# Kernel tuning notes

Measured on AMD Instinct MI355X. Metric: run time of the kernel, lower is better.

## Reference

```python
import jax, jax.numpy as jnp
import numpy as np

B, L, C = 4, 4096, 2048
NH, K = 32, 16
F = C // NH  # head_dim = 64
LR = 1.0     # config.inner_net_lr
EPS = 1e-6


def setup_inputs() -> dict:
    key = jax.random.key(0)
    ks = jax.random.split(key, 8)
    s = 0.02
    return {
        "hidden_states": jax.random.normal(ks[0], (B, L, C), jnp.float32),
        "q_w": jax.random.normal(ks[1], (C, C), jnp.float32) * s,
        "k_w": jax.random.normal(ks[2], (C, C), jnp.float32) * s,
        "v_w": jax.random.normal(ks[3], (C, C), jnp.float32) * s,
        "o_w": jax.random.normal(ks[4], (C, C), jnp.float32) * s,
        "lin_w": jax.random.normal(ks[5], (NH, 1, C), jnp.float32) * s,
        "lin_b": jnp.zeros((NH, 1), jnp.float32),
        "ln_w": jnp.ones((NH, F), jnp.float32),
        "ln_b": jnp.zeros((NH, F), jnp.float32),
        "W1": jax.random.normal(ks[6], (NH, F, F), jnp.float32) * s,
        "b1": jnp.zeros((NH, 1, F), jnp.float32),
    }


def _ln(z, g, b):
    # LayerNormFunction.forward over last dim (head_dim)
    mu = z.mean(-1, keepdims=True)
    var = jnp.mean((z - mu) ** 2, axis=-1, keepdims=True)
    x_hat = (z - mu) * jax.lax.rsqrt(var + EPS)
    return g * x_hat + b


def _ln_l2_bwd(z, target, g, b):
    # decoder_ln_bwd: grad of 0.5*||LN(z) - target||^2 w.r.t. z, fused LN fwd+bwd
    mu = z.mean(-1, keepdims=True)
    var = jnp.mean((z - mu) ** 2, axis=-1, keepdims=True)
    std = jnp.sqrt(var + EPS)
    x_hat = (z - mu) / std
    gy = (g * x_hat + b - target) * g  # grad_x_hat
    return (F * gy - gy.sum(-1, keepdims=True)
            - x_hat * (gy * x_hat).sum(-1, keepdims=True)) / (F * std)


def reference(hidden_states, q_w, k_w, v_w, o_w, lin_w, lin_b, ln_w, ln_b, W1, b1):
    nc = L // K  # number of inner chunks

    def proj(w):
        x = hidden_states @ w.T                      # [B,L,C]
        x = x.reshape(B, nc, K, NH, F)
        return jnp.moveaxis(x, 3, 1)                 # [B,NH,nc,K,F]

    XC, XB, XA = proj(q_w), proj(k_w), proj(v_w)

    # per-head ilr gate: vmap(F.linear) over heads, softplus activation
    Xr = hidden_states.reshape(B, nc, K, C)
    ilr = jax.nn.softplus(jnp.einsum('bnkc,hoc->bhnko', Xr, lin_w)
                          + lin_b[None, :, None, None, :])   # [B,NH,nc,K,1]
    token_idx = 1.0 / jnp.arange(1, K + 1, dtype=jnp.float32)
    coeff = (LR * token_idx)[None, None, None, :, None] * ilr / F  # [B,NH,nc,K,1]

    gamma = ln_w[None, :, None, :]  # [1,NH,1,F]
    beta = ln_b[None, :, None, :]
    mask = jnp.tril(jnp.ones((K, K), jnp.float32))

    W1_0 = jnp.broadcast_to(W1[None], (B, NH, F, F))
    b1_0 = jnp.broadcast_to(b1[None], (B, NH, 1, F))

    def step(carry, xs):
        W1s, b1s = carry
        xa, xb, xc, co = xs                 # [B,NH,K,F], co: [B,NH,K,1]
        Z1 = xb @ W1s + b1s                 # inner-net forward
        gZ = _ln_l2_bwd(Z1, xa - xb, gamma, beta)  # grad_l_wrt_Z1
        Attn1 = (xc @ jnp.swapaxes(xb, -1, -2)) * mask      # tril(XC XB^T) [B,NH,K,K]
        b1_bar = b1s - (co * mask) @ gZ                      # [B,NH,K,F]
        Z1_bar = xc @ W1s - (co * Attn1) @ gZ + b1_bar       # dual-form output
        co_last = co[:, :, -1:, :]                           # [B,NH,1,1]
        W1_new = W1s - jnp.swapaxes(co_last * xb, -1, -2) @ gZ
        b1_new = b1_bar[:, :, -1:, :]
        xcw = xc + _ln(Z1_bar, gamma, beta)
        return (W1_new, b1_new), xcw

    xs = tuple(jnp.moveaxis(t, 2, 0) for t in (XA, XB, XC, coeff))
    _, out = jax.lax.scan(step, (W1_0, b1_0), xs)   # out: [nc,B,NH,K,F]
    out = jnp.moveaxis(out, 0, 1)                    # [B,nc,NH,K,F]
    out = jnp.swapaxes(out, 2, 3).reshape(B, L, C)   # [B,L,C]
    return out @ o_w.T
```

## Files before the change

### kernel.cpp

```cpp
#include <hip/hip_runtime.h>
#include <hip/hip_bf16.h>

#define B_ 4
#define L_ 4096
#define C_ 2048
#define NH_ 32
#define K_ 16
#define F_ 64
#define NC_ 256
#define EPS_ 1e-6f

typedef _Float16 half8 __attribute__((ext_vector_type(8)));
typedef _Float16 half4 __attribute__((ext_vector_type(4)));
typedef float f32x4 __attribute__((ext_vector_type(4)));

__device__ __forceinline__ float red16(float v) {
  int x;
  x = __builtin_amdgcn_update_dpp(0, __builtin_bit_cast(int, v), 0xB1, 0xF, 0xF, true);
  v += __builtin_bit_cast(float, x);
  x = __builtin_amdgcn_update_dpp(0, __builtin_bit_cast(int, v), 0x4E, 0xF, 0xF, true);
  v += __builtin_bit_cast(float, x);
  x = __builtin_amdgcn_update_dpp(0, __builtin_bit_cast(int, v), 0x124, 0xF, 0xF, true);
  v += __builtin_bit_cast(float, x);
  x = __builtin_amdgcn_update_dpp(0, __builtin_bit_cast(int, v), 0x128, 0xF, 0xF, true);
  v += __builtin_bit_cast(float, x);
  return v;
}

__device__ __forceinline__ void gl_lds16(const _Float16* g, _Float16* l) {
  __builtin_amdgcn_global_load_lds(
      (const __attribute__((address_space(1))) void*)g,
      (__attribute__((address_space(3))) void*)l, 16, 0, 0);
}

__global__ __launch_bounds__(256) void cast_f16(const float* __restrict__ in,
                                                _Float16* __restrict__ out, int n8) {
  int i = blockIdx.x * 256 + threadIdx.x;
  if (i >= n8) return;
  const float4* ip = (const float4*)in;
  float4 a = ip[2*i], b = ip[2*i+1];
  half8 o;
  o[0]=(_Float16)a.x; o[1]=(_Float16)a.y; o[2]=(_Float16)a.z; o[3]=(_Float16)a.w;
  o[4]=(_Float16)b.x; o[5]=(_Float16)b.y; o[6]=(_Float16)b.z; o[7]=(_Float16)b.w;
  ((half8*)out)[i] = o;
}

#define GBM2 256
#define GBN2 256
#define GBK2 32

template<typename OT>
__global__ __launch_bounds__(512) void gemm_f16_v2(
    const _Float16* __restrict__ A, const _Float16* __restrict__ Bm,
    OT* __restrict__ C, int M, int N, int Kd)
{
  __shared__ __align__(16) _Float16 As[3][GBM2*GBK2];
  __shared__ __align__(16) _Float16 Bs[3][GBM2*GBK2];
  const int t = threadIdx.x;
  const int lane = t & 63;
  const int w = t >> 6;
  const int bn = blockIdx.x, bm = blockIdx.y;
  const int wm = (w >> 2) * 128;
  const int wn = (w & 3) * 64;
  const int ln = lane & 15, q = lane >> 4;

  const _Float16* gA0 = A  + ((long)(bm*GBM2 +        (t>>2)))*Kd + (t&3)*8;
  const _Float16* gA1 = A  + ((long)(bm*GBM2 + 128 +  (t>>2)))*Kd + (t&3)*8;
  const _Float16* gB0 = Bm + ((long)(bn*GBN2 +        (t>>2)))*Kd + (t&3)*8;
  const _Float16* gB1 = Bm + ((long)(bn*GBN2 + 128 +  (t>>2)))*Kd + (t&3)*8;

  auto stage = [&](int tile, int bi) {
    const long off = (long)tile * GBK2;
    gl_lds16(gA0 + off, &As[bi][(size_t)t*8]);
    gl_lds16(gA1 + off, &As[bi][(size_t)(t+512)*8]);
    gl_lds16(gB0 + off, &Bs[bi][(size_t)t*8]);
    gl_lds16(gB1 + off, &Bs[bi][(size_t)(t+512)*8]);
  };

  f32x4 acc[8][4];
#pragma unroll
  for (int i = 0; i < 8; ++i)
#pragma unroll
    for (int j = 0; j < 4; ++j) acc[i][j] = (f32x4){0.f,0.f,0.f,0.f};

  auto compute = [&](int kt) {
    const _Float16* as = As[kt % 3];
    const _Float16* bs = Bs[kt % 3];
    half8 bf[4];
#pragma unroll
    for (int ni = 0; ni < 4; ++ni)
      bf[ni] = *(const half8*)(bs + (size_t)(wn + ni*16 + ln)*GBK2 + q*8);
    __builtin_amdgcn_s_setprio(1);
#pragma unroll
    for (int mi = 0; mi < 8; ++mi) {
      half8 af = *(const half8*)(as + (size_t)(wm + mi*16 + ln)*GBK2 + q*8);
#pragma unroll
      for (int ni = 0; ni < 4; ++ni)
        acc[mi][ni] = __builtin_amdgcn_mfma_f32_16x16x32_f16(af, bf[ni], acc[mi][ni], 0, 0, 0);
    }
    __builtin_amdgcn_s_setprio(0);
  };

  const int NT = Kd / GBK2;
  stage(0, 0);
  stage(1, 1);

  for (int kt = 0; kt < NT - 2; ++kt) {
    __builtin_amdgcn_sched_barrier(0);
    __builtin_amdgcn_s_barrier();
    __builtin_amdgcn_sched_barrier(0);
    stage(kt + 2, (kt + 2) % 3);
    __builtin_amdgcn_sched_barrier(0);
    asm volatile("s_waitcnt vmcnt(8)" ::: "memory");
    __builtin_amdgcn_sched_barrier(0);
    compute(kt);
  }
  __builtin_amdgcn_sched_barrier(0);
  __builtin_amdgcn_s_barrier();
  __builtin_amdgcn_sched_barrier(0);
  asm volatile("s_waitcnt vmcnt(4)" ::: "memory");
  __builtin_amdgcn_sched_barrier(0);
  compute(NT - 2);
  __builtin_amdgcn_sched_barrier(0);
  __builtin_amdgcn_s_barrier();
  __builtin_amdgcn_sched_barrier(0);
  asm volatile("s_waitcnt vmcnt(0)" ::: "memory");
  __builtin_amdgcn_sched_barrier(0);
  compute(NT - 1);

  const int cr = q * 4, cc = ln;
#pragma unroll
  for (int mi = 0; mi < 8; ++mi)
#pragma unroll
    for (int ni = 0; ni < 4; ++ni)
#pragma unroll
      for (int r = 0; r < 4; ++r) {
        long row = (long)bm*GBM2 + wm + mi*16 + cr + r;
        long col = (long)bn*GBN2 + wn + ni*16 + cc;
        C[row*(long)N + col] = (OT)acc[mi][ni][r];
      }
}

__global__ __launch_bounds__(256) void ilr_kernel(
    const float* __restrict__ hid, const float* __restrict__ lin_w,
    const float* __restrict__ lin_b, float* __restrict__ coeff)
{
  const int t = threadIdx.x;
  const int lane = t & 63;
  const int w = t >> 6;
  const int row0 = blockIdx.x * 16 + w * 4;

  float4 hv[4][8];
#pragma unroll
  for (int r = 0; r < 4; ++r) {
    const float* hp = hid + (size_t)(row0 + r) * C_;
#pragma unroll
    for (int i = 0; i < 8; ++i) hv[r][i] = *(const float4*)(hp + i*256 + lane*4);
  }
  float res[4] = {0.f,0.f,0.f,0.f};
  for (int h = 0; h < NH_; ++h) {
    const float* wp = lin_w + (size_t)h * C_;
    float s[4] = {0.f,0.f,0.f,0.f};
#pragma unroll
    for (int i = 0; i < 8; ++i) {
      float4 wv = *(const float4*)(wp + i*256 + lane*4);
#pragma unroll
      for (int r = 0; r < 4; ++r)
        s[r] += hv[r][i].x*wv.x + hv[r][i].y*wv.y + hv[r][i].z*wv.z + hv[r][i].w*wv.w;
    }
#pragma unroll
    for (int o = 32; o > 0; o >>= 1)
#pragma unroll
      for (int r = 0; r < 4; ++r) s[r] += __shfl_xor(s[r], o, 64);
    if (lane == h) { res[0]=s[0]; res[1]=s[1]; res[2]=s[2]; res[3]=s[3]; }
  }
  if (lane < NH_) {
    float lb = lin_b[lane];
#pragma unroll
    for (int r = 0; r < 4; ++r) {
      int row = row0 + r;
      int b = row >> 12;
      int li = row & (L_ - 1);
      int k = li & (K_ - 1);
      float x = res[r] + lb;
      float sp = (x > 20.f) ? x : log1pf(expf(x));
      float v = (1.0f / (float)(k + 1)) * sp * (1.0f / (float)F_);
      coeff[((size_t)(b * NH_ + lane)) * L_ + li] = v;
    }
  }
}

struct Ck2 {
  half4 xbA[4], xsA[4];
  float co4[4], co15;
};

__device__ __forceinline__ void load_ck2(
    Ck2& c, const _Float16* Kp, const _Float16* S, const float* co,
    size_t rowbase, int hoff, size_t cobase, int n, int q, int ln)
{
#pragma unroll
  for (int kt = 0; kt < 4; ++kt) {
    size_t idx = (rowbase + ln) * C_ + hoff + 16*kt + 4*q;
    c.xbA[kt] = *(const half4*)(Kp + idx);
    c.xsA[kt] = *(const half4*)(S  + idx);
  }
#pragma unroll
  for (int r = 0; r < 4; ++r) c.co4[r] = co[cobase + (size_t)n*K_ + 4*q + r];
  c.co15 = co[cobase + (size_t)n*K_ + 15];
}

__global__ __launch_bounds__(128, 1) void scan_kernel(
    const _Float16* __restrict__ Q, const _Float16* __restrict__ Kp,
    const _Float16* __restrict__ V,
    const float* __restrict__ coeff, const float* __restrict__ W1g, const float* __restrict__ b1g,
    const float* __restrict__ ln_w, const float* __restrict__ ln_b,
    _Float16* __restrict__ OF)
{
  const int bh = blockIdx.x;
  const int b = bh >> 5, h = bh & 31;
  const int tid = threadIdx.x;
  const int lane = tid & 63;
  const bool isP = tid < 64;
  const int q = lane >> 4, ln = lane & 15;
  const int hoff = h * F_;
  const size_t cobase = (size_t)bh * L_;
  const size_t brow = (size_t)b * L_;

  __shared__ half4 gzs[4][4][64];

  half4 W1f[4][4];
#pragma unroll
  for (int kt = 0; kt < 4; ++kt)
#pragma unroll
    for (int t = 0; t < 4; ++t) {
      half4 hv;
#pragma unroll
      for (int j = 0; j < 4; ++j)
        hv[j] = (_Float16)W1g[(size_t)h*F_*F_ + (size_t)(16*kt + 4*q + j)*F_ + 16*t + ln];
      W1f[kt][t] = hv;
    }
  float b1r[4], gamt[4], bett[4];
#pragma unroll
  for (int t = 0; t < 4; ++t) {
    b1r[t]  = b1g[hoff + 16*t + ln];
    gamt[t] = ln_w[hoff + 16*t + ln];
    bett[t] = ln_b[hoff + 16*t + ln];
  }
  half4 maskA, maskI;
#pragma unroll
  for (int j = 0; j < 4; ++j) {
    maskA[j] = (_Float16)((4*q + j <= ln) ? 1.f : 0.f);
    maskI[j] = (_Float16)((4*q + j == ln) ? 1.f : 0.f);
  }
  const f32x4 zf4 = (f32x4){0.f, 0.f, 0.f, 0.f};

  const _Float16* S = isP ? V : Q;

  auto iter = [&](int i, Ck2& cur, Ck2& nxt) {
    half4 gzf[4];
    half4 xbTp[4];
    float co15p = 0.f;

    if (isP) {
      if (i < NC_) {
        co15p = cur.co15;
        if (i + 1 < NC_)
          load_ck2(nxt, Kp, S, coeff, brow + (size_t)(i+1)*K_, hoff, cobase, i+1, q, ln);
        f32x4 tgD[4];
#pragma unroll
        for (int t = 0; t < 4; ++t) {
          half4 dd = cur.xsA[t] - cur.xbA[t];
          tgD[t] = __builtin_amdgcn_mfma_f32_16x16x16f16(dd, maskI, zf4, 0, 0, 0);
          f32x4 x = __builtin_amdgcn_mfma_f32_16x16x16f16(cur.xbA[t], maskI, zf4, 0, 0, 0);
          half4 v;
#pragma unroll
          for (int r = 0; r < 4; ++r) v[r] = (_Float16)x[r];
          xbTp[t] = v;
        }
        f32x4 za[4];
#pragma unroll
        for (int t = 0; t < 4; ++t) {
          f32x4 zh = (f32x4){b1r[t], b1r[t], b1r[t], b1r[t]};
#pragma unroll
          for (int kt = 0; kt < 4; ++kt)
            zh = __builtin_amdgcn_mfma_f32_16x16x16f16(cur.xbA[kt], W1f[kt][t], zh, 0, 0, 0);
          za[t] = zh;
        }
#pragma unroll
        for (int r = 0; r < 4; ++r) {
          float zr[4], s1 = 0.f, s2 = 0.f;
#pragma unroll
          for (int t = 0; t < 4; ++t) { zr[t] = za[t][r]; s1 += zr[t]; s2 += zr[t]*zr[t]; }
          s1 = red16(s1); s2 = red16(s2);
          float mu = s1 * (1.f/F_);
          float istd = rsqrtf(s2 * (1.f/F_) - mu*mu + EPS_);
          float xh[4], gy[4], sg = 0.f, sx = 0.f;
#pragma unroll
          for (int t = 0; t < 4; ++t) {
            xh[t] = (zr[t] - mu) * istd;
            gy[t] = (gamt[t]*xh[t] + bett[t] - tgD[t][r]) * gamt[t];
            sg += gy[t]; sx += gy[t]*xh[t];
          }
          sg = red16(sg); sx = red16(sx);
          const float sc = istd * (1.f/F_);
#pragma unroll
          for (int t = 0; t < 4; ++t)
            gzf[t][r] = (_Float16)((F_*gy[t] - sg - xh[t]*sx) * sc);
        }
#pragma unroll
        for (int t = 0; t < 4; ++t) gzs[i & 3][t][lane] = gzf[t];
      }
    } else {
      if (i < NC_)
        load_ck2(nxt, Kp, S, coeff, brow + (size_t)i*K_, hoff, cobase, i, q, ln);
    }

    __syncthreads();

    if (isP) {
      if (i < NC_) {
        f32x4 cum3[4];
#pragma unroll
        for (int t = 0; t < 4; ++t)
          cum3[t] = __builtin_amdgcn_mfma_f32_16x16x16f16(maskA, gzf[t], zf4, 0, 0, 0);
#pragma unroll
        for (int t = 0; t < 4; ++t) {
          float tmp = b1r[t] - co15p * cum3[t][3];
          b1r[t] = __shfl(tmp, 48 + ln, 64);
        }
#pragma unroll
        for (int mt = 0; mt < 4; ++mt)
#pragma unroll
          for (int t = 0; t < 4; ++t) {
            f32x4 d = __builtin_amdgcn_mfma_f32_16x16x16f16(xbTp[mt], gzf[t], zf4, 0, 0, 0);
            half4 dt;
#pragma unroll
            for (int r = 0; r < 4; ++r) dt[r] = (_Float16)(co15p * d[r]);
            W1f[mt][t] = W1f[mt][t] - dt;
          }
      }
    } else {
      if (i > 0) {
        const int jc = i - 1;
        const size_t rowbase = brow + (size_t)jc * K_;
        half4 gz[4];
#pragma unroll
        for (int t = 0; t < 4; ++t) gz[t] = gzs[jc & 3][t][lane];
        f32x4 xcsD[4]; half4 xbT[4];
#pragma unroll
        for (int t = 0; t < 4; ++t) {
          xcsD[t] = __builtin_amdgcn_mfma_f32_16x16x16f16(cur.xsA[t], maskI, zf4, 0, 0, 0);
          f32x4 x = __builtin_amdgcn_mfma_f32_16x16x16f16(cur.xbA[t], maskI, zf4, 0, 0, 0);
          half4 v;
#pragma unroll
          for (int r = 0; r < 4; ++r) v[r] = (_Float16)x[r];
          xbT[t] = v;
        }
        f32x4 at0 = zf4, at1 = zf4;
        at0 = __builtin_amdgcn_mfma_f32_16x16x16f16(cur.xbA[0], cur.xsA[0], at0, 0, 0, 0);
        at0 = __builtin_amdgcn_mfma_f32_16x16x16f16(cur.xbA[1], cur.xsA[1], at0, 0, 0, 0);
        at1 = __builtin_amdgcn_mfma_f32_16x16x16f16(cur.xbA[2], cur.xsA[2], at1, 0, 0, 0);
        at1 = __builtin_amdgcn_mfma_f32_16x16x16f16(cur.xbA[3], cur.xsA[3], at1, 0, 0, 0);
        f32x4 at = at0 + at1;
        half4 atf;
#pragma unroll
        for (int r = 0; r < 4; ++r) atf[r] = (_Float16)((4*q + r <= ln) ? at[r] : 0.f);
        f32x4 cum[4], ag[4];
#pragma unroll
        for (int t = 0; t < 4; ++t) {
          cum[t] = __builtin_amdgcn_mfma_f32_16x16x16f16(maskA, gz[t], zf4, 0, 0, 0);
          ag[t]  = __builtin_amdgcn_mfma_f32_16x16x16f16(atf,   gz[t], zf4, 0, 0, 0);
        }
        float zbf[4][4];
#pragma unroll
        for (int t = 0; t < 4; ++t) {
          f32x4 zh = zf4;
#pragma unroll
          for (int kt = 0; kt < 4; ++kt)
            zh = __builtin_amdgcn_mfma_f32_16x16x16f16(cur.xsA[kt], W1f[kt][t], zh, 0, 0, 0);
#pragma unroll
          for (int r = 0; r < 4; ++r)
            zbf[t][r] = zh[r] + b1r[t] - cur.co4[r]*(ag[t][r] + cum[t][r]);
        }
#pragma unroll
        for (int r = 0; r < 4; ++r) {
          float zr[4], s1 = 0.f, s2 = 0.f;
#pragma unroll
          for (int t = 0; t < 4; ++t) { zr[t] = zbf[t][r]; s1 += zr[t]; s2 += zr[t]*zr[t]; }
          s1 = red16(s1); s2 = red16(s2);
          float mu = s1 * (1.f/F_);
          float istd = rsqrtf(s2 * (1.f/F_) - mu*mu + EPS_);
#pragma unroll
          for (int t = 0; t < 4; ++t) {
            float ov = xcsD[t][r] + gamt[t]*((zr[t] - mu)*istd) + bett[t];
            OF[(rowbase + 4*q + r) * C_ + hoff + 16*t + ln] = (_Float16)ov;
          }
        }
#pragma unroll
        for (int t = 0; t < 4; ++t) {
          float tmp = b1r[t] - cur.co15 * cum[t][3];
          b1r[t] = __shfl(tmp, 48 + ln, 64);
        }
#pragma unroll
        for (int mt = 0; mt < 4; ++mt)
#pragma unroll
          for (int t = 0; t < 4; ++t) {
            f32x4 d = __builtin_amdgcn_mfma_f32_16x16x16f16(xbT[mt], gz[t], zf4, 0, 0, 0);
            half4 dt;
#pragma unroll
            for (int r = 0; r < 4; ++r) dt[r] = (_Float16)(cur.co15 * d[r]);
            W1f[mt][t] = W1f[mt][t] - dt;
          }
      }
    }
  };

  Ck2 cka, ckb;
  if (isP) load_ck2(cka, Kp, S, coeff, brow, hoff, cobase, 0, q, ln);

  for (int i = 0; i < NC_; i += 2) {
    iter(i,     cka, ckb);
    iter(i + 1, ckb, cka);
  }
  iter(NC_, cka, ckb);
}

extern "C" void kernel_launch(void* const* d_in, const int* in_sizes, int n_in,
                              void* d_out, int out_size, void* d_ws, size_t ws_size,
                              hipStream_t stream)
{
  const float* hid   = (const float*)d_in[0];
  const float* q_w   = (const float*)d_in[1];
  const float* k_w   = (const float*)d_in[2];
  const float* v_w   = (const float*)d_in[3];
  const float* o_w   = (const float*)d_in[4];
  const float* lin_w = (const float*)d_in[5];
  const float* lin_b = (const float*)d_in[6];
  const float* ln_w  = (const float*)d_in[7];
  const float* ln_b  = (const float*)d_in[8];
  const float* W1    = (const float*)d_in[9];
  const float* b1    = (const float*)d_in[10];
  float* out = (float*)d_out;

  const size_t BLC = (size_t)B_ * L_ * C_;
  const size_t CC  = (size_t)C_ * C_;
  _Float16* HF = (_Float16*)d_ws;
  _Float16* WF = HF + BLC;
  _Float16* KF = WF + CC;
  _Float16* VF = KF + BLC;
  float*    CO = (float*)(VF + BLC);
  _Float16* QF = (_Float16*)d_out;

  const int M = B_ * L_, N = C_, Kd = C_;
  dim3 gg2(N / GBN2, M / GBM2);
  const int n8h = (int)(BLC / 8);
  const int n8w = (int)(CC / 8);

  cast_f16<<<(n8h+255)/256, 256, 0, stream>>>(hid, HF, n8h);
  cast_f16<<<(n8w+255)/256, 256, 0, stream>>>(q_w, WF, n8w);
  gemm_f16_v2<_Float16><<<gg2, 512, 0, stream>>>(HF, WF, QF, M, N, Kd);
  cast_f16<<<(n8w+255)/256, 256, 0, stream>>>(k_w, WF, n8w);
  gemm_f16_v2<_Float16><<<gg2, 512, 0, stream>>>(HF, WF, KF, M, N, Kd);
  cast_f16<<<(n8w+255)/256, 256, 0, stream>>>(v_w, WF, n8w);
  gemm_f16_v2<_Float16><<<gg2, 512, 0, stream>>>(HF, WF, VF, M, N, Kd);
  ilr_kernel<<<M / 16, 256, 0, stream>>>(hid, lin_w, lin_b, CO);
  scan_kernel<<<B_ * NH_, 128, 0, stream>>>(QF, KF, VF, CO, W1, b1, ln_w, ln_b, HF);
  cast_f16<<<(n8w+255)/256, 256, 0, stream>>>(o_w, WF, n8w);
  gemm_f16_v2<float><<<gg2, 512, 0, stream>>>(HF, WF, out, M, N, Kd);
}
```

Baseline: 1.379 ms.

## Fuse QKV projections into one GEMM with BK=64 swizzled double-buffered pipeline

Concatenates the three fp16-cast projection weights and runs a single GEMM over a 3x-wide N grid, routing each column block to the Q, K or V output. The GEMM kernel moves from a triple-buffered BK=32 loop to a double-buffered BK=64 loop with XOR-swizzled LDS layout, split staging interleaved between MFMA phases, and a launch bound requesting two blocks per CU. The aim is fewer launches, a larger grid for better CU fill, fewer LDS bank conflicts and better overlap of loads with compute. In exchange it costs more workspace for the concatenated weights, and the higher occupancy target may cause register pressure.

```diff
diff --git a/kernel.cpp b/kernel.cpp
--- a/kernel.cpp
+++ b/kernel.cpp
@@ -45,37 +45,37 @@
   ((half8*)out)[i] = o;
 }
 
-#define GBM2 256
-#define GBN2 256
-#define GBK2 32
+#define BM3 256
+#define BN3 256
+#define BK3 64
 
 template<typename OT>
-__global__ __launch_bounds__(512) void gemm_f16_v2(
+__global__ __launch_bounds__(512, 2) void gemm_f16_v3(
     const _Float16* __restrict__ A, const _Float16* __restrict__ Bm,
-    OT* __restrict__ C, int M, int N, int Kd)
+    OT* __restrict__ C0, OT* __restrict__ C1, OT* __restrict__ C2, int Kd)
 {
-  __shared__ __align__(16) _Float16 As[3][GBM2*GBK2];
-  __shared__ __align__(16) _Float16 Bs[3][GBM2*GBK2];
+  __shared__ __align__(16) _Float16 As[2][2][128*64];
+  __shared__ __align__(16) _Float16 Bs[2][2][128*64];
   const int t = threadIdx.x;
   const int lane = t & 63;
   const int w = t >> 6;
+  const int wr = w >> 2, wc = w & 3;
   const int bn = blockIdx.x, bm = blockIdx.y;
-  const int wm = (w >> 2) * 128;
-  const int wn = (w & 3) * 64;
   const int ln = lane & 15, q = lane >> 4;
 
-  const _Float16* gA0 = A  + ((long)(bm*GBM2 +        (t>>2)))*Kd + (t&3)*8;
-  const _Float16* gA1 = A  + ((long)(bm*GBM2 + 128 +  (t>>2)))*Kd + (t&3)*8;
-  const _Float16* gB0 = Bm + ((long)(bn*GBN2 +        (t>>2)))*Kd + (t&3)*8;
-  const _Float16* gB1 = Bm + ((long)(bn*GBN2 + 128 +  (t>>2)))*Kd + (t&3)*8;
-
-  auto stage = [&](int tile, int bi) {
-    const long off = (long)tile * GBK2;
-    gl_lds16(gA0 + off, &As[bi][(size_t)t*8]);
-    gl_lds16(gA1 + off, &As[bi][(size_t)(t+512)*8]);
-    gl_lds16(gB0 + off, &Bs[bi][(size_t)t*8]);
-    gl_lds16(gB1 + off, &Bs[bi][(size_t)(t+512)*8]);
+  const int srow = t >> 3, sc = t & 7;
+  const int clg = sc ^ (2 * ((srow >> 2) & 1));
+
+  auto stageA = [&](int kt, int h, int db) {
+    const _Float16* g = A + ((long)(bm*BM3 + h*128 + srow))*Kd + (long)kt*BK3 + clg*8;
+    gl_lds16(g,          &As[db][h][(size_t)srow*64 + sc*8]);
+    gl_lds16(g + 64*Kd,  &As[db][h][(size_t)(64+srow)*64 + sc*8]);
   };
+  auto stageB = [&](int kt, int h, int db) {
+    const _Float16* g = Bm + ((long)(bn*BN3 + h*128 + srow))*Kd + (long)kt*BK3 + clg*8;
+    gl_lds16(g,          &Bs[db][h][(size_t)srow*64 + sc*8]);
+    gl_lds16(g + 64*Kd,  &Bs[db][h][(size_t)(64+srow)*64 + sc*8]);
+  };
 
   f32x4 acc[8][4];
 #pragma unroll
@@ -83,61 +83,117 @@
 #pragma unroll
     for (int j = 0; j < 4; ++j) acc[i][j] = (f32x4){0.f,0.f,0.f,0.f};
 
-  auto compute = [&](int kt) {
-    const _Float16* as = As[kt % 3];
-    const _Float16* bs = Bs[kt % 3];
-    half8 bf[4];
-#pragma unroll
-    for (int ni = 0; ni < 4; ++ni)
-      bf[ni] = *(const half8*)(bs + (size_t)(wn + ni*16 + ln)*GBK2 + q*8);
-    __builtin_amdgcn_s_setprio(1);
-#pragma unroll
-    for (int mi = 0; mi < 8; ++mi) {
-      half8 af = *(const half8*)(as + (size_t)(wm + mi*16 + ln)*GBK2 + q*8);
-#pragma unroll
-      for (int ni = 0; ni < 4; ++ni)
-        acc[mi][ni] = __builtin_amdgcn_mfma_f32_16x16x32_f16(af, bf[ni], acc[mi][ni], 0, 0, 0);
-    }
-    __builtin_amdgcn_s_setprio(0);
-  };
-
-  const int NT = Kd / GBK2;
-  stage(0, 0);
-  stage(1, 1);
-
-  for (int kt = 0; kt < NT - 2; ++kt) {
+  half8 af[8][2], bf[4][2];
+
+  stageA(0, 0, 0); stageA(0, 1, 0); stageB(0, 0, 0); stageB(0, 1, 0);
+
+  const int NT = Kd / BK3;
+  for (int kt = 0; kt < NT; ++kt) {
+    const int db = kt & 1;
+    const bool more = (kt + 1 < NT);
+    if (more) { stageA(kt+1, 0, db^1); stageB(kt+1, 0, db^1); }
+    __builtin_amdgcn_sched_barrier(0);
+    if (more) asm volatile("s_waitcnt vmcnt(4)" ::: "memory");
+    else      asm volatile("s_waitcnt vmcnt(0)" ::: "memory");
     __builtin_amdgcn_sched_barrier(0);
     __builtin_amdgcn_s_barrier();
     __builtin_amdgcn_sched_barrier(0);
-    stage(kt + 2, (kt + 2) % 3);
+
+    const _Float16* ap = &As[db][wr][0];
+    const _Float16* bp = &Bs[db][wc >> 1][0];
+    const int lcb = (wc & 1) * 64;
+
+#pragma unroll
+    for (int mi = 0; mi < 4; ++mi)
+#pragma unroll
+      for (int ks = 0; ks < 2; ++ks) {
+        int lr = mi*16 + ln;
+        int cp = (ks*4 + q) ^ (2*((lr>>2)&1));
+        af[mi][ks] = *(const half8*)(ap + (size_t)lr*64 + cp*8);
+      }
+#pragma unroll
+    for (int ni = 0; ni < 2; ++ni)
+#pragma unroll
+      for (int ks = 0; ks < 2; ++ks) {
+        int lc = lcb + ni*16 + ln;
+        int cp = (ks*4 + q) ^ (2*((lc>>2)&1));
+        bf[ni][ks] = *(const half8*)(bp + (size_t)lc*64 + cp*8);
+      }
+    __builtin_amdgcn_s_setprio(1);
+#pragma unroll
+    for (int mi = 0; mi < 4; ++mi)
+#pragma unroll
+      for (int ni = 0; ni < 2; ++ni)
+#pragma unroll
+        for (int ks = 0; ks < 2; ++ks)
+          acc[mi][ni] = __builtin_amdgcn_mfma_f32_16x16x32_f16(af[mi][ks], bf[ni][ks], acc[mi][ni], 0, 0, 0);
+    __builtin_amdgcn_s_setprio(0);
+    if (more) stageA(kt+1, 1, db^1);
+
+#pragma unroll
+    for (int mi = 4; mi < 8; ++mi)
+#pragma unroll
+      for (int ks = 0; ks < 2; ++ks) {
+        int lr = mi*16 + ln;
+        int cp = (ks*4 + q) ^ (2*((lr>>2)&1));
+        af[mi][ks] = *(const half8*)(ap + (size_t)lr*64 + cp*8);
+      }
+    __builtin_amdgcn_s_setprio(1);
+#pragma unroll
+    for (int mi = 4; mi < 8; ++mi)
+#pragma unroll
+      for (int ni = 0; ni < 2; ++ni)
+#pragma unroll
+        for (int ks = 0; ks < 2; ++ks)
+          acc[mi][ni] = __builtin_amdgcn_mfma_f32_16x16x32_f16(af[mi][ks], bf[ni][ks], acc[mi][ni], 0, 0, 0);
+    __builtin_amdgcn_s_setprio(0);
+    if (more) stageB(kt+1, 1, db^1);
+
+#pragma unroll
+    for (int ni = 2; ni < 4; ++ni)
+#pragma unroll
+      for (int ks = 0; ks < 2; ++ks) {
+        int lc = lcb + ni*16 + ln;
+        int cp = (ks*4 + q) ^ (2*((lc>>2)&1));
+        bf[ni][ks] = *(const half8*)(bp + (size_t)lc*64 + cp*8);
+      }
+    __builtin_amdgcn_s_setprio(1);
+#pragma unroll
+    for (int mi = 4; mi < 8; ++mi)
+#pragma unroll
+      for (int ni = 2; ni < 4; ++ni)
+#pragma unroll
+        for (int ks = 0; ks < 2; ++ks)
+          acc[mi][ni] = __builtin_amdgcn_mfma_f32_16x16x32_f16(af[mi][ks], bf[ni][ks], acc[mi][ni], 0, 0, 0);
+    __builtin_amdgcn_s_setprio(0);
+
+    __builtin_amdgcn_s_setprio(1);
+#pragma unroll
+    for (int mi = 0; mi < 4; ++mi)
+#pragma unroll
+      for (int ni = 2; ni < 4; ++ni)
+#pragma unroll
+        for (int ks = 0; ks < 2; ++ks)
+          acc[mi][ni] = __builtin_amdgcn_mfma_f32_16x16x32_f16(af[mi][ks], bf[ni][ks], acc[mi][ni], 0, 0, 0);
+    __builtin_amdgcn_s_setprio(0);
+
     __builtin_amdgcn_sched_barrier(0);
-    asm volatile("s_waitcnt vmcnt(8)" ::: "memory");
+    __builtin_amdgcn_s_barrier();
     __builtin_amdgcn_sched_barrier(0);
-    compute(kt);
-  }
-  __builtin_amdgcn_sched_barrier(0);
-  __builtin_amdgcn_s_barrier();
-  __builtin_amdgcn_sched_barrier(0);
-  asm volatile("s_waitcnt vmcnt(4)" ::: "memory");
-  __builtin_amdgcn_sched_barrier(0);
-  compute(NT - 2);
-  __builtin_amdgcn_sched_barrier(0);
-  __builtin_amdgcn_s_barrier();
-  __builtin_amdgcn_sched_barrier(0);
-  asm volatile("s_waitcnt vmcnt(0)" ::: "memory");
-  __builtin_amdgcn_sched_barrier(0);
-  compute(NT - 1);
-
-  const int cr = q * 4, cc = ln;
+  }
+
+  const int reg = bn >> 3, bnl = bn & 7;
+  OT* C = (reg == 0) ? C0 : ((reg == 1) ? C1 : C2);
+  const int cr = q * 4;
 #pragma unroll
   for (int mi = 0; mi < 8; ++mi)
 #pragma unroll
     for (int ni = 0; ni < 4; ++ni)
 #pragma unroll
       for (int r = 0; r < 4; ++r) {
-        long row = (long)bm*GBM2 + wm + mi*16 + cr + r;
-        long col = (long)bn*GBN2 + wn + ni*16 + cc;
-        C[row*(long)N + col] = (OT)acc[mi][ni][r];
+        long row = (long)bm*BM3 + wr*128 + mi*16 + cr + r;
+        long col = (long)bnl*256 + wc*64 + ni*16 + ln;
+        C[row*2048L + col] = (OT)acc[mi][ni][r];
       }
 }
 
@@ -445,27 +501,26 @@
 
   const size_t BLC = (size_t)B_ * L_ * C_;
   const size_t CC  = (size_t)C_ * C_;
-  _Float16* HF = (_Float16*)d_ws;
-  _Float16* WF = HF + BLC;
-  _Float16* KF = WF + CC;
-  _Float16* VF = KF + BLC;
-  float*    CO = (float*)(VF + BLC);
-  _Float16* QF = (_Float16*)d_out;
-
-  const int M = B_ * L_, N = C_, Kd = C_;
-  dim3 gg2(N / GBN2, M / GBM2);
+  _Float16* HF  = (_Float16*)d_ws;
+  _Float16* WF3 = HF + BLC;
+  _Float16* KF  = WF3 + 3*CC;
+  _Float16* VF  = KF + BLC;
+  float*    CO  = (float*)(VF + BLC);
+  _Float16* QF  = (_Float16*)d_out;
+
+  const int M = B_ * L_, Kd = C_;
+  dim3 ggQKV(3 * C_ / BN3, M / BM3);
+  dim3 ggO(C_ / BN3, M / BM3);
   const int n8h = (int)(BLC / 8);
   const int n8w = (int)(CC / 8);
 
   cast_f16<<<(n8h+255)/256, 256, 0, stream>>>(hid, HF, n8h);
-  cast_f16<<<(n8w+255)/256, 256, 0, stream>>>(q_w, WF, n8w);
-  gemm_f16_v2<_Float16><<<gg2, 512, 0, stream>>>(HF, WF, QF, M, N, Kd);
-  cast_f16<<<(n8w+255)/256, 256, 0, stream>>>(k_w, WF, n8w);
-  gemm_f16_v2<_Float16><<<gg2, 512, 0, stream>>>(HF, WF, KF, M, N, Kd);
-  cast_f16<<<(n8w+255)/256, 256, 0, stream>>>(v_w, WF, n8w);
-  gemm_f16_v2<_Float16><<<gg2, 512, 0, stream>>>(HF, WF, VF, M, N, Kd);
+  cast_f16<<<(n8w+255)/256, 256, 0, stream>>>(q_w, WF3,        n8w);
+  cast_f16<<<(n8w+255)/256, 256, 0, stream>>>(k_w, WF3 + CC,   n8w);
+  cast_f16<<<(n8w+255)/256, 256, 0, stream>>>(v_w, WF3 + 2*CC, n8w);
+  gemm_f16_v3<_Float16><<<ggQKV, 512, 0, stream>>>(HF, WF3, QF, KF, VF, Kd);
   ilr_kernel<<<M / 16, 256, 0, stream>>>(hid, lin_w, lin_b, CO);
   scan_kernel<<<B_ * NH_, 128, 0, stream>>>(QF, KF, VF, CO, W1, b1, ln_w, ln_b, HF);
-  cast_f16<<<(n8w+255)/256, 256, 0, stream>>>(o_w, WF, n8w);
-  gemm_f16_v2<float><<<gg2, 512, 0, stream>>>(HF, WF, out, M, N, Kd);
-}
+  cast_f16<<<(n8w+255)/256, 256, 0, stream>>>(o_w, WF3, n8w);
+  gemm_f16_v3<float><<<ggO, 512, 0, stream>>>(HF, WF3, out, out, out, Kd);
+}
```

After: 1.293 ms. 6.2% less time.
